# Optimization experiments

Measured on AMD Instinct MI355X. Metric: run time of the kernel, lower is better.

The kernel has to match this reference:

```python
import jax, jax.numpy as jnp
import numpy as np

N = 100000
E = 600000
F_IN = 128
HID = 256
C = 64


def setup_inputs() -> dict:
    key = jax.random.key(0)
    ks = jax.random.split(key, 6)
    x = jax.random.normal(ks[0], (N, F_IN), dtype=jnp.float32)
    edge_index = jax.random.randint(ks[1], (2, E), 0, N, dtype=jnp.int64)
    W1 = jax.random.normal(ks[2], (F_IN, HID), dtype=jnp.float32) * (1.0 / np.sqrt(F_IN))
    b1 = jnp.zeros((HID,), dtype=jnp.float32)
    W2 = jax.random.normal(ks[3], (HID, C), dtype=jnp.float32) * (1.0 / np.sqrt(HID))
    b2 = jnp.zeros((C,), dtype=jnp.float32)
    return {"x": x, "W1": W1, "b1": b1, "W2": W2, "b2": b2, "edge_index": edge_index}


def _gcn_conv(h, W, b, src, dst, norm, self_w):
    # h: [N, F_in] -> [N, F_out]; symmetric-normalized aggregation over A+I
    h = h @ W  # [N, F_out]
    agg = jax.ops.segment_sum(h[src] * norm[:, None], dst, num_segments=N)
    agg = agg + h * self_w[:, None]  # self-loop contribution d^{-1/2}*d^{-1/2}
    return agg + b


def reference(x, W1, b1, W2, b2, edge_index):
    src, dst = edge_index[0], edge_index[1]
    # degree of A + I (self-loops added): 1 + in-degree
    deg = jnp.ones((N,), dtype=x.dtype).at[dst].add(1.0)
    dinv = jax.lax.rsqrt(deg)
    norm = dinv[src] * dinv[dst]  # [E]
    self_w = dinv * dinv          # [N]

    h = _gcn_conv(x, W1, b1, src, dst, norm, self_w)
    h = jax.nn.relu(h)
    # dropout is identity in eval mode (training=False)
    out = _gcn_conv(h, W2, b2, src, dst, norm, self_w)
    return jax.nn.log_softmax(out, axis=1)
```

## Files before the change

### kernel.cpp

```cpp
#include <hip/hip_runtime.h>
#include <cstdint>
#include <cstddef>

#define N_NODES 100000
#define N_EDGES 600000
#define F_IN    128
#define HID     256
#define NC      64
#define NB_SCAN 391

typedef __attribute__((ext_vector_type(8))) short bf16x8;
typedef __attribute__((ext_vector_type(4))) float f32x4;

__device__ __forceinline__ unsigned short f2bf(float f) {
    unsigned int u = __float_as_uint(f);
    u = (u + 0x7FFFu + ((u >> 16) & 1u)) >> 16;
    return (unsigned short)u;
}
__device__ __forceinline__ float bf2f(unsigned short u) {
    return __uint_as_float(((unsigned int)u) << 16);
}

__global__ void k_detect(const int* __restrict__ ei_words, int* __restrict__ mode) {
    if (blockIdx.x == 0 && threadIdx.x == 0) {
        int allz = 1;
        for (int i = 0; i < 64; ++i) {
            long long s = (long long)i * (N_EDGES - 1) / 63;
            if (ei_words[2 * s + 1] != 0) { allz = 0; break; }
        }
        *mode = allz;
    }
}

__device__ __forceinline__ int load_idx(const void* ei, int m, long long i) {
    return m ? (int)((const long long*)ei)[i] : ((const int*)ei)[i];
}

__global__ void k_zero(int* __restrict__ p, int n) {
    int i = blockIdx.x * blockDim.x + threadIdx.x;
    if (i < n) p[i] = 0;
}

__global__ void k_hist(const void* __restrict__ ei, const int* __restrict__ mode,
                       int* __restrict__ deg) {
    int e = blockIdx.x * blockDim.x + threadIdx.x;
    if (e >= N_EDGES) return;
    int d = load_idx(ei, *mode, (long long)N_EDGES + e);
    atomicAdd(&deg[d], 1);
}

__global__ void k_scanA(const int* __restrict__ deg, int* __restrict__ ptmp,
                        int* __restrict__ bsum) {
    __shared__ int sm[256];
    int i = blockIdx.x * 256 + threadIdx.x;
    int v = (i < N_NODES) ? deg[i] : 0;
    sm[threadIdx.x] = v;
    __syncthreads();
    for (int off = 1; off < 256; off <<= 1) {
        int t = (threadIdx.x >= off) ? sm[threadIdx.x - off] : 0;
        __syncthreads();
        sm[threadIdx.x] += t;
        __syncthreads();
    }
    if (i < N_NODES) ptmp[i] = sm[threadIdx.x] - v;
    if (threadIdx.x == 255) bsum[blockIdx.x] = sm[255];
}

__global__ void k_scanB(int* __restrict__ bsum) {
    __shared__ int sm[512];
    int i = threadIdx.x;
    int v = (i < NB_SCAN) ? bsum[i] : 0;
    sm[i] = v;
    __syncthreads();
    for (int off = 1; off < 512; off <<= 1) {
        int t = (i >= off) ? sm[i - off] : 0;
        __syncthreads();
        sm[i] += t;
        __syncthreads();
    }
    if (i < NB_SCAN) bsum[i] = sm[i] - v;
}

__global__ void k_scanC(const int* __restrict__ deg, const int* __restrict__ ptmp,
                        const int* __restrict__ bsum, int* __restrict__ row_ptr,
                        int* __restrict__ cursor, float* __restrict__ dinv) {
    int i = blockIdx.x * 256 + threadIdx.x;
    if (i < N_NODES) {
        int rp = ptmp[i] + bsum[blockIdx.x];
        row_ptr[i] = rp;
        cursor[i]  = rp;
        dinv[i]    = rsqrtf(1.0f + (float)deg[i]);
    }
    if (i == 0) row_ptr[N_NODES] = N_EDGES;
}

__global__ void k_fill(const void* __restrict__ ei, const int* __restrict__ mode,
                       int* __restrict__ cursor, int* __restrict__ csr_src) {
    int e = blockIdx.x * blockDim.x + threadIdx.x;
    if (e >= N_EDGES) return;
    int m = *mode;
    int s = load_idx(ei, m, e);
    int d = load_idx(ei, m, (long long)N_EDGES + e);
    int pos = atomicAdd(&cursor[d], 1);
    csr_src[pos] = s;
}

__global__ void k_w1t(const float* __restrict__ W1, unsigned short* __restrict__ W1T) {
    int i = blockIdx.x * 256 + threadIdx.x;
    int k = i >> 8, n = i & 255;
    W1T[n * F_IN + k] = f2bf(W1[i]);
}
__global__ void k_w2t(const float* __restrict__ W2, unsigned short* __restrict__ W2T) {
    int i = blockIdx.x * 256 + threadIdx.x;
    int k = i >> 6, n = i & 63;
    W2T[n * HID + k] = f2bf(W2[i]);
}

__global__ void k_xbf(const float* __restrict__ x, unsigned short* __restrict__ xbf) {
    int i = blockIdx.x * 256 + threadIdx.x;
    const float4* xr = (const float4*)x;
    float4 a = xr[(size_t)i * 2];
    float4 b = xr[(size_t)i * 2 + 1];
    bf16x8 o;
    o[0] = (short)f2bf(a.x); o[1] = (short)f2bf(a.y);
    o[2] = (short)f2bf(a.z); o[3] = (short)f2bf(a.w);
    o[4] = (short)f2bf(b.x); o[5] = (short)f2bf(b.y);
    o[6] = (short)f2bf(b.z); o[7] = (short)f2bf(b.w);
    *(bf16x8*)(xbf + (size_t)i * 8) = o;
}

__global__ void k_gather1(const unsigned short* __restrict__ xbf,
                          const int* __restrict__ row_ptr,
                          const int* __restrict__ csr_src, const float* __restrict__ dinv,
                          unsigned short* __restrict__ px) {
    int g = threadIdx.x >> 4;
    int j = threadIdx.x & 15;
    int n = blockIdx.x * 16 + g;
    float dn = dinv[n];
    bf16x8 sv = *(const bf16x8*)(xbf + (size_t)n * F_IN + j * 8);
    float acc[8];
#pragma unroll
    for (int t = 0; t < 8; ++t) acc[t] = bf2f((unsigned short)sv[t]) * dn;
    int e0 = row_ptr[n], e1 = row_ptr[n + 1];
    for (int k = e0; k < e1; ++k) {
        int s = csr_src[k];
        float w = dinv[s];
        bf16x8 v = *(const bf16x8*)(xbf + (size_t)s * F_IN + j * 8);
#pragma unroll
        for (int t = 0; t < 8; ++t)
            acc[t] = fmaf(bf2f((unsigned short)v[t]), w, acc[t]);
    }
    bf16x8 o;
#pragma unroll
    for (int t = 0; t < 8; ++t) o[t] = (short)f2bf(acc[t] * dn);
    *(bf16x8*)(px + (size_t)n * F_IN + j * 8) = o;
}

__global__ __launch_bounds__(256) void k_gemm1_mfma(
        const unsigned short* __restrict__ px, const unsigned short* __restrict__ W1T,
        const float* __restrict__ b1, unsigned short* __restrict__ h) {
    const int lane = threadIdx.x & 63;
    const int w    = threadIdx.x >> 6;
    const int l15  = lane & 15, lhi = lane >> 4;
    const int row0 = blockIdx.x * 64;
    const int col0 = w * 64;

    f32x4 acc[4][4];
#pragma unroll
    for (int mt = 0; mt < 4; ++mt)
#pragma unroll
        for (int nt = 0; nt < 4; ++nt) acc[mt][nt] = (f32x4){0.f, 0.f, 0.f, 0.f};

#pragma unroll
    for (int ks = 0; ks < 4; ++ks) {
        bf16x8 a[4];
#pragma unroll
        for (int mt = 0; mt < 4; ++mt)
            a[mt] = *(const bf16x8*)(px + (size_t)(row0 + mt * 16 + l15) * F_IN + ks * 32 + lhi * 8);
#pragma unroll
        for (int nt = 0; nt < 4; ++nt) {
            bf16x8 b = *(const bf16x8*)(W1T + (size_t)(col0 + nt * 16 + l15) * F_IN + ks * 32 + lhi * 8);
#pragma unroll
            for (int mt = 0; mt < 4; ++mt)
                acc[mt][nt] = __builtin_amdgcn_mfma_f32_16x16x32_bf16(b, a[mt], acc[mt][nt], 0, 0, 0);
        }
    }

#pragma unroll
    for (int mt = 0; mt < 4; ++mt) {
        const int r = row0 + mt * 16 + l15;
        if (r < N_NODES) {
#pragma unroll
            for (int nt = 0; nt < 4; ++nt) {
                int c0 = col0 + nt * 16 + lhi * 4;
                float4 bb = *(const float4*)(b1 + c0);
                ushort4 o;
                o.x = f2bf(fmaxf(acc[mt][nt][0] + bb.x, 0.f));
                o.y = f2bf(fmaxf(acc[mt][nt][1] + bb.y, 0.f));
                o.z = f2bf(fmaxf(acc[mt][nt][2] + bb.z, 0.f));
                o.w = f2bf(fmaxf(acc[mt][nt][3] + bb.w, 0.f));
                *(ushort4*)(h + (size_t)r * HID + c0) = o;
            }
        }
    }
}

__global__ __launch_bounds__(256) void k_gemm2_mfma(
        const unsigned short* __restrict__ h, const unsigned short* __restrict__ W2T,
        float* __restrict__ hx2) {
    const int lane = threadIdx.x & 63;
    const int w    = threadIdx.x >> 6;
    const int l15  = lane & 15, lhi = lane >> 4;
    const int row0 = blockIdx.x * 256 + w * 64;

    f32x4 acc[4][4];
#pragma unroll
    for (int mt = 0; mt < 4; ++mt)
#pragma unroll
        for (int nt = 0; nt < 4; ++nt) acc[mt][nt] = (f32x4){0.f, 0.f, 0.f, 0.f};

#pragma unroll
    for (int ks = 0; ks < 8; ++ks) {
        bf16x8 a[4];
#pragma unroll
        for (int mt = 0; mt < 4; ++mt)
            a[mt] = *(const bf16x8*)(h + (size_t)(row0 + mt * 16 + l15) * HID + ks * 32 + lhi * 8);
#pragma unroll
        for (int nt = 0; nt < 4; ++nt) {
            bf16x8 b = *(const bf16x8*)(W2T + (size_t)(nt * 16 + l15) * HID + ks * 32 + lhi * 8);
#pragma unroll
            for (int mt = 0; mt < 4; ++mt)
                acc[mt][nt] = __builtin_amdgcn_mfma_f32_16x16x32_bf16(b, a[mt], acc[mt][nt], 0, 0, 0);
        }
    }

#pragma unroll
    for (int mt = 0; mt < 4; ++mt) {
        const int r = row0 + mt * 16 + l15;
        if (r < N_NODES) {
#pragma unroll
            for (int nt = 0; nt < 4; ++nt) {
                int c0 = nt * 16 + lhi * 4;
                float4 o = make_float4(acc[mt][nt][0], acc[mt][nt][1],
                                       acc[mt][nt][2], acc[mt][nt][3]);
                *(float4*)(hx2 + (size_t)r * NC + c0) = o;
            }
        }
    }
}

__global__ void k_gather2sm(const float* __restrict__ hx2, const int* __restrict__ row_ptr,
                            const int* __restrict__ csr_src, const float* __restrict__ dinv,
                            const float* __restrict__ b2, float* __restrict__ out) {
    int g = threadIdx.x >> 4;
    int j = threadIdx.x & 15;
    int n = blockIdx.x * 16 + g;
    float dn = dinv[n];
    const float4* hr = (const float4*)hx2;
    float4 a = hr[(size_t)n * 16 + j];
    float4 acc;
    acc.x = a.x * dn; acc.y = a.y * dn; acc.z = a.z * dn; acc.w = a.w * dn;
    int e0 = row_ptr[n], e1 = row_ptr[n + 1];
    for (int k = e0; k < e1; ++k) {
        int s = csr_src[k];
        float w = dinv[s];
        float4 v = hr[(size_t)s * 16 + j];
        acc.x = fmaf(v.x, w, acc.x); acc.y = fmaf(v.y, w, acc.y);
        acc.z = fmaf(v.z, w, acc.z); acc.w = fmaf(v.w, w, acc.w);
    }
    const float4 b = ((const float4*)b2)[j];
    float4 o;
    o.x = fmaf(acc.x, dn, b.x); o.y = fmaf(acc.y, dn, b.y);
    o.z = fmaf(acc.z, dn, b.z); o.w = fmaf(acc.w, dn, b.w);
    float mx = fmaxf(fmaxf(o.x, o.y), fmaxf(o.z, o.w));
#pragma unroll
    for (int msk = 8; msk; msk >>= 1) mx = fmaxf(mx, __shfl_xor(mx, msk));
    float s4 = expf(o.x - mx) + expf(o.y - mx) + expf(o.z - mx) + expf(o.w - mx);
#pragma unroll
    for (int msk = 8; msk; msk >>= 1) s4 += __shfl_xor(s4, msk);
    float ls = mx + logf(s4);
    o.x -= ls; o.y -= ls; o.z -= ls; o.w -= ls;
    ((float4*)out)[(size_t)n * 16 + j] = o;
}

extern "C" void kernel_launch(void* const* d_in, const int* in_sizes, int n_in,
                              void* d_out, int out_size, void* d_ws, size_t ws_size,
                              hipStream_t stream) {
    const float* x  = (const float*)d_in[0];
    const float* W1 = (const float*)d_in[1];
    const float* b1 = (const float*)d_in[2];
    const float* W2 = (const float*)d_in[3];
    const float* b2 = (const float*)d_in[4];
    const void*  ei = d_in[5];
    float* out = (float*)d_out;

    char* ws = (char*)d_ws;
    size_t off = 0;
    auto alloc = [&](size_t bytes) {
        char* p = ws + off;
        off += (bytes + 255) & ~(size_t)255;
        return p;
    };
    int*            mode    = (int*)            alloc(4);
    int*            deg     = (int*)            alloc((size_t)N_NODES * 4);
    int*            ptmp    = (int*)            alloc((size_t)N_NODES * 4);
    int*            bsum    = (int*)            alloc(4096);
    int*            row_ptr = (int*)            alloc((size_t)(N_NODES + 1) * 4);
    int*            cursor  = (int*)            alloc((size_t)N_NODES * 4);
    float*          dinv    = (float*)          alloc((size_t)N_NODES * 4);
    int*            csr_src = (int*)            alloc((size_t)N_EDGES * 4);
    unsigned short* W1T     = (unsigned short*) alloc((size_t)F_IN * HID * 2);
    unsigned short* W2T     = (unsigned short*) alloc((size_t)HID * NC * 2);
    unsigned short* xbf     = (unsigned short*) alloc((size_t)N_NODES * F_IN * 2);
    unsigned short* px      = (unsigned short*) alloc((size_t)(N_NODES + 64) * F_IN * 2);
    unsigned short* h       = (unsigned short*) alloc((size_t)(N_NODES + 128) * HID * 2);
    float*          hx2     = (float*)          alloc((size_t)N_NODES * NC * 4);

    k_detect<<<1, 64, 0, stream>>>((const int*)ei, mode);

    k_zero<<<(N_NODES + 255) / 256, 256, 0, stream>>>(deg, N_NODES);
    k_hist<<<(N_EDGES + 255) / 256, 256, 0, stream>>>(ei, mode, deg);
    k_scanA<<<NB_SCAN, 256, 0, stream>>>(deg, ptmp, bsum);
    k_scanB<<<1, 512, 0, stream>>>(bsum);
    k_scanC<<<NB_SCAN, 256, 0, stream>>>(deg, ptmp, bsum, row_ptr, cursor, dinv);
    k_fill<<<(N_EDGES + 255) / 256, 256, 0, stream>>>(ei, mode, cursor, csr_src);

    k_w1t<<<F_IN * HID / 256, 256, 0, stream>>>(W1, W1T);
    k_w2t<<<HID * NC / 256, 256, 0, stream>>>(W2, W2T);
    k_xbf<<<N_NODES * F_IN / 8 / 256, 256, 0, stream>>>(x, xbf);

    k_gather1<<<N_NODES / 16, 256, 0, stream>>>(xbf, row_ptr, csr_src, dinv, px);
    k_gemm1_mfma<<<(N_NODES + 63) / 64, 256, 0, stream>>>(px, W1T, b1, h);

    k_gemm2_mfma<<<(N_NODES + 255) / 256, 256, 0, stream>>>(h, W2T, hx2);
    k_gather2sm<<<N_NODES / 16, 256, 0, stream>>>(hx2, row_ptr, csr_src, dinv, b2, out);
}
```

Before: 227.2 us.

## Fuse both GEMMs through LDS and store layer-2 features as bf16

Merges the first GEMM (with bias and ReLU) and the second GEMM into one kernel that keeps the 64x256 hidden tile in XOR-swizzled shared memory, so the N x 256 hidden matrix never goes to global memory. The second-layer projection is now written as bf16 instead of fp32, which halves the bytes the final neighbor gather reads. The cost is 32 KB of LDS per block, which limits occupancy, plus extra rounding error in the layer-2 features.

```diff
diff --git a/kernel.cpp b/kernel.cpp
--- a/kernel.cpp
+++ b/kernel.cpp
@@ -156,40 +156,42 @@
     *(bf16x8*)(px + (size_t)n * F_IN + j * 8) = o;
 }
 
-__global__ __launch_bounds__(256) void k_gemm1_mfma(
+__global__ __launch_bounds__(256) void k_mlp_fused(
         const unsigned short* __restrict__ px, const unsigned short* __restrict__ W1T,
-        const float* __restrict__ b1, unsigned short* __restrict__ h) {
+        const float* __restrict__ b1, const unsigned short* __restrict__ W2T,
+        unsigned short* __restrict__ hx2) {
+    __shared__ unsigned short hlds[64 * HID];
     const int lane = threadIdx.x & 63;
     const int w    = threadIdx.x >> 6;
     const int l15  = lane & 15, lhi = lane >> 4;
     const int row0 = blockIdx.x * 64;
-    const int col0 = w * 64;
-
-    f32x4 acc[4][4];
-#pragma unroll
-    for (int mt = 0; mt < 4; ++mt)
-#pragma unroll
-        for (int nt = 0; nt < 4; ++nt) acc[mt][nt] = (f32x4){0.f, 0.f, 0.f, 0.f};
-
-#pragma unroll
-    for (int ks = 0; ks < 4; ++ks) {
-        bf16x8 a[4];
+
+    {
+        const int col0 = w * 64;
+        f32x4 acc[4][4];
 #pragma unroll
         for (int mt = 0; mt < 4; ++mt)
-            a[mt] = *(const bf16x8*)(px + (size_t)(row0 + mt * 16 + l15) * F_IN + ks * 32 + lhi * 8);
-#pragma unroll
-        for (int nt = 0; nt < 4; ++nt) {
-            bf16x8 b = *(const bf16x8*)(W1T + (size_t)(col0 + nt * 16 + l15) * F_IN + ks * 32 + lhi * 8);
+#pragma unroll
+            for (int nt = 0; nt < 4; ++nt) acc[mt][nt] = (f32x4){0.f, 0.f, 0.f, 0.f};
+
+#pragma unroll
+        for (int ks = 0; ks < 4; ++ks) {
+            bf16x8 a[4];
 #pragma unroll
             for (int mt = 0; mt < 4; ++mt)
-                acc[mt][nt] = __builtin_amdgcn_mfma_f32_16x16x32_bf16(b, a[mt], acc[mt][nt], 0, 0, 0);
-        }
-    }
-
-#pragma unroll
-    for (int mt = 0; mt < 4; ++mt) {
-        const int r = row0 + mt * 16 + l15;
-        if (r < N_NODES) {
+                a[mt] = *(const bf16x8*)(px + (size_t)(row0 + mt * 16 + l15) * F_IN + ks * 32 + lhi * 8);
+#pragma unroll
+            for (int nt = 0; nt < 4; ++nt) {
+                bf16x8 b = *(const bf16x8*)(W1T + (size_t)(col0 + nt * 16 + l15) * F_IN + ks * 32 + lhi * 8);
+#pragma unroll
+                for (int mt = 0; mt < 4; ++mt)
+                    acc[mt][nt] = __builtin_amdgcn_mfma_f32_16x16x32_bf16(b, a[mt], acc[mt][nt], 0, 0, 0);
+            }
+        }
+
+#pragma unroll
+        for (int mt = 0; mt < 4; ++mt) {
+            const int lr = mt * 16 + l15;
 #pragma unroll
             for (int nt = 0; nt < 4; ++nt) {
                 int c0 = col0 + nt * 16 + lhi * 4;
@@ -199,79 +201,70 @@
                 o.y = f2bf(fmaxf(acc[mt][nt][1] + bb.y, 0.f));
                 o.z = f2bf(fmaxf(acc[mt][nt][2] + bb.z, 0.f));
                 o.w = f2bf(fmaxf(acc[mt][nt][3] + bb.w, 0.f));
-                *(ushort4*)(h + (size_t)r * HID + c0) = o;
+                unsigned byte = (unsigned)(lr * (HID * 2) + c0 * 2) ^ ((lr & 7) << 4);
+                *(ushort4*)((char*)hlds + byte) = o;
             }
         }
     }
-}
-
-__global__ __launch_bounds__(256) void k_gemm2_mfma(
-        const unsigned short* __restrict__ h, const unsigned short* __restrict__ W2T,
-        float* __restrict__ hx2) {
-    const int lane = threadIdx.x & 63;
-    const int w    = threadIdx.x >> 6;
-    const int l15  = lane & 15, lhi = lane >> 4;
-    const int row0 = blockIdx.x * 256 + w * 64;
-
-    f32x4 acc[4][4];
-#pragma unroll
-    for (int mt = 0; mt < 4; ++mt)
-#pragma unroll
-        for (int nt = 0; nt < 4; ++nt) acc[mt][nt] = (f32x4){0.f, 0.f, 0.f, 0.f};
-
-#pragma unroll
-    for (int ks = 0; ks < 8; ++ks) {
-        bf16x8 a[4];
-#pragma unroll
-        for (int mt = 0; mt < 4; ++mt)
-            a[mt] = *(const bf16x8*)(h + (size_t)(row0 + mt * 16 + l15) * HID + ks * 32 + lhi * 8);
+    __syncthreads();
+
+    {
+        const int lr = w * 16 + l15;
+        bf16x8 a2[8];
+#pragma unroll
+        for (int ks = 0; ks < 8; ++ks) {
+            unsigned byte = (unsigned)(lr * (HID * 2) + ks * 64 + lhi * 16) ^ ((lr & 7) << 4);
+            a2[ks] = *(const bf16x8*)((const char*)hlds + byte);
+        }
+        f32x4 acc2[4];
+#pragma unroll
+        for (int nt = 0; nt < 4; ++nt) acc2[nt] = (f32x4){0.f, 0.f, 0.f, 0.f};
 #pragma unroll
         for (int nt = 0; nt < 4; ++nt) {
-            bf16x8 b = *(const bf16x8*)(W2T + (size_t)(nt * 16 + l15) * HID + ks * 32 + lhi * 8);
-#pragma unroll
-            for (int mt = 0; mt < 4; ++mt)
-                acc[mt][nt] = __builtin_amdgcn_mfma_f32_16x16x32_bf16(b, a[mt], acc[mt][nt], 0, 0, 0);
-        }
-    }
-
-#pragma unroll
-    for (int mt = 0; mt < 4; ++mt) {
-        const int r = row0 + mt * 16 + l15;
+            const unsigned short* pb = W2T + (size_t)(nt * 16 + l15) * HID + lhi * 8;
+#pragma unroll
+            for (int ks = 0; ks < 8; ++ks) {
+                bf16x8 b = *(const bf16x8*)(pb + ks * 32);
+                acc2[nt] = __builtin_amdgcn_mfma_f32_16x16x32_bf16(b, a2[ks], acc2[nt], 0, 0, 0);
+            }
+        }
+        const int r = row0 + lr;
         if (r < N_NODES) {
 #pragma unroll
             for (int nt = 0; nt < 4; ++nt) {
                 int c0 = nt * 16 + lhi * 4;
-                float4 o = make_float4(acc[mt][nt][0], acc[mt][nt][1],
-                                       acc[mt][nt][2], acc[mt][nt][3]);
-                *(float4*)(hx2 + (size_t)r * NC + c0) = o;
+                ushort4 o;
+                o.x = f2bf(acc2[nt][0]); o.y = f2bf(acc2[nt][1]);
+                o.z = f2bf(acc2[nt][2]); o.w = f2bf(acc2[nt][3]);
+                *(ushort4*)(hx2 + (size_t)r * NC + c0) = o;
             }
         }
     }
 }
 
-__global__ void k_gather2sm(const float* __restrict__ hx2, const int* __restrict__ row_ptr,
+__global__ void k_gather2sm(const unsigned short* __restrict__ hx2,
+                            const int* __restrict__ row_ptr,
                             const int* __restrict__ csr_src, const float* __restrict__ dinv,
                             const float* __restrict__ b2, float* __restrict__ out) {
     int g = threadIdx.x >> 4;
     int j = threadIdx.x & 15;
     int n = blockIdx.x * 16 + g;
     float dn = dinv[n];
-    const float4* hr = (const float4*)hx2;
-    float4 a = hr[(size_t)n * 16 + j];
-    float4 acc;
-    acc.x = a.x * dn; acc.y = a.y * dn; acc.z = a.z * dn; acc.w = a.w * dn;
+    ushort4 sv = *(const ushort4*)(hx2 + (size_t)n * NC + j * 4);
+    float ax = bf2f(sv.x) * dn, ay = bf2f(sv.y) * dn,
+          az = bf2f(sv.z) * dn, aw = bf2f(sv.w) * dn;
     int e0 = row_ptr[n], e1 = row_ptr[n + 1];
     for (int k = e0; k < e1; ++k) {
         int s = csr_src[k];
-        float w = dinv[s];
-        float4 v = hr[(size_t)s * 16 + j];
-        acc.x = fmaf(v.x, w, acc.x); acc.y = fmaf(v.y, w, acc.y);
-        acc.z = fmaf(v.z, w, acc.z); acc.w = fmaf(v.w, w, acc.w);
+        float wv = dinv[s];
+        ushort4 v = *(const ushort4*)(hx2 + (size_t)s * NC + j * 4);
+        ax = fmaf(bf2f(v.x), wv, ax); ay = fmaf(bf2f(v.y), wv, ay);
+        az = fmaf(bf2f(v.z), wv, az); aw = fmaf(bf2f(v.w), wv, aw);
     }
     const float4 b = ((const float4*)b2)[j];
     float4 o;
-    o.x = fmaf(acc.x, dn, b.x); o.y = fmaf(acc.y, dn, b.y);
-    o.z = fmaf(acc.z, dn, b.z); o.w = fmaf(acc.w, dn, b.w);
+    o.x = fmaf(ax, dn, b.x); o.y = fmaf(ay, dn, b.y);
+    o.z = fmaf(az, dn, b.z); o.w = fmaf(aw, dn, b.w);
     float mx = fmaxf(fmaxf(o.x, o.y), fmaxf(o.z, o.w));
 #pragma unroll
     for (int msk = 8; msk; msk >>= 1) mx = fmaxf(mx, __shfl_xor(mx, msk));
@@ -313,8 +306,7 @@
     unsigned short* W2T     = (unsigned short*) alloc((size_t)HID * NC * 2);
     unsigned short* xbf     = (unsigned short*) alloc((size_t)N_NODES * F_IN * 2);
     unsigned short* px      = (unsigned short*) alloc((size_t)(N_NODES + 64) * F_IN * 2);
-    unsigned short* h       = (unsigned short*) alloc((size_t)(N_NODES + 128) * HID * 2);
-    float*          hx2     = (float*)          alloc((size_t)N_NODES * NC * 4);
+    unsigned short* hx2     = (unsigned short*) alloc((size_t)(N_NODES + 64) * NC * 2);
 
     k_detect<<<1, 64, 0, stream>>>((const int*)ei, mode);
 
@@ -330,8 +322,6 @@
     k_xbf<<<N_NODES * F_IN / 8 / 256, 256, 0, stream>>>(x, xbf);
 
     k_gather1<<<N_NODES / 16, 256, 0, stream>>>(xbf, row_ptr, csr_src, dinv, px);
-    k_gemm1_mfma<<<(N_NODES + 63) / 64, 256, 0, stream>>>(px, W1T, b1, h);
-
-    k_gemm2_mfma<<<(N_NODES + 255) / 256, 256, 0, stream>>>(h, W2T, hx2);
+    k_mlp_fused<<<(N_NODES + 63) / 64, 256, 0, stream>>>(px, W1T, b1, W2T, hx2);
     k_gather2sm<<<N_NODES / 16, 256, 0, stream>>>(hx2, row_ptr, csr_src, dinv, b2, out);
 }
```

New measurement: 220.1 us. 1.03x faster.
